# Kernel optimization log

Measured on AMD Instinct MI355X. Metric: run time of the kernel, lower is better.

The kernel has to match this reference:

```python
import jax, jax.numpy as jnp
import numpy as np

NUM_SHARED = 2
NUM_EXPERTS = 8
NUM_LOCAL = NUM_EXPERTS - NUM_SHARED
TOP_K = 2
BALANCE_COEFF = 0.1
INPUT_DIM = 256
HIDDEN_DIM = 512
PRED_LEN = 256
NUM_SCALES = 3


def _gelu(v):
    return jax.nn.gelu(v, approximate=False)  # torch nn.GELU default = exact erf


def setup_inputs() -> dict:
    key = jax.random.key(0)
    ks = iter(jax.random.split(key, 32))
    s = 0.02

    def w(shape):
        return jax.random.normal(next(ks), shape, dtype=jnp.float32) * s

    inp = {}
    inp["xs"] = jax.random.normal(next(ks), (NUM_SCALES, 32, 512, INPUT_DIM), dtype=jnp.float32)
    # router: Linear(E, 2E) -> GELU -> Linear(2E, num_experts) -> softmax
    inp["router_w1"] = w((INPUT_DIM, 2 * INPUT_DIM)); inp["router_b1"] = jnp.zeros((2 * INPUT_DIM,), jnp.float32)
    inp["router_w2"] = w((2 * INPUT_DIM, NUM_EXPERTS)); inp["router_b2"] = jnp.zeros((NUM_EXPERTS,), jnp.float32)
    # global experts (3-layer MLP), stacked over num_shared
    inp["gW1"] = w((NUM_SHARED, INPUT_DIM, HIDDEN_DIM)); inp["gb1"] = jnp.zeros((NUM_SHARED, HIDDEN_DIM), jnp.float32)
    inp["gW2"] = w((NUM_SHARED, HIDDEN_DIM, HIDDEN_DIM)); inp["gb2"] = jnp.zeros((NUM_SHARED, HIDDEN_DIM), jnp.float32)
    inp["gW3"] = w((NUM_SHARED, HIDDEN_DIM, PRED_LEN)); inp["gb3"] = jnp.zeros((NUM_SHARED, PRED_LEN), jnp.float32)
    # local experts (2-layer MLP), stacked over num_local
    inp["lW1"] = w((NUM_LOCAL, INPUT_DIM, HIDDEN_DIM)); inp["lb1"] = jnp.zeros((NUM_LOCAL, HIDDEN_DIM), jnp.float32)
    inp["lW2"] = w((NUM_LOCAL, HIDDEN_DIM, PRED_LEN)); inp["lb2"] = jnp.zeros((NUM_LOCAL, PRED_LEN), jnp.float32)
    # TemporalAwareWeighting
    inp["te_w"] = w((PRED_LEN, PRED_LEN)); inp["te_b"] = jnp.zeros((PRED_LEN,), jnp.float32)
    inp["weight_memory"] = jnp.zeros((1, NUM_SCALES), jnp.float32)
    inp["wc_w"] = w((PRED_LEN * NUM_SCALES + NUM_SCALES, NUM_SCALES)); inp["wc_b"] = jnp.zeros((NUM_SCALES,), jnp.float32)
    # output layer
    inp["out_w1"] = w((PRED_LEN, PRED_LEN)); inp["out_b1"] = jnp.zeros((PRED_LEN,), jnp.float32)
    inp["out_w2"] = w((PRED_LEN, PRED_LEN)); inp["out_b2"] = jnp.zeros((PRED_LEN,), jnp.float32)
    return inp


def reference(xs, router_w1, router_b1, router_w2, router_b2,
              gW1, gb1, gW2, gb2, gW3, gb3,
              lW1, lb1, lW2, lb2,
              te_w, te_b, weight_memory, wc_w, wc_b,
              out_w1, out_b1, out_w2, out_b2):
    S, B, C, E = xs.shape
    x = xs.reshape(S, B * C, E)

    def scale_fwd(xf):  # xf: [T, E]
        h = _gelu(xf @ router_w1 + router_b1)
        w = jax.nn.softmax(h @ router_w2 + router_b2, axis=-1)  # [T, Ne]
        gw = w[:, :NUM_SHARED]
        lw, lidx = jax.lax.top_k(w[:, NUM_SHARED:], TOP_K)      # sorted desc, like torch.topk
        # global experts: all run, weighted sum
        gh = _gelu(jnp.einsum('te,seh->sth', xf, gW1) + gb1[:, None, :])
        gh = _gelu(jnp.einsum('sth,shg->stg', gh, gW2) + gb2[:, None, :])
        gout = jnp.einsum('stg,sgo->sto', gh, gW3) + gb3[:, None, :]   # [Ns, T, O]
        global_pred = jnp.einsum('sto,ts->to', gout, gw)
        # local experts: all run (as in source), then top-k gather
        lh = _gelu(jnp.einsum('te,neh->nth', xf, lW1) + lb1[:, None, :])
        lout = jnp.einsum('nth,nho->nto', lh, lW2) + lb2[:, None, :]   # [Nl, T, O]
        sel = jnp.take_along_axis(jnp.swapaxes(lout, 0, 1), lidx[:, :, None], axis=1)  # [T, k, O]
        local_pred = jnp.sum(sel * lw[:, :, None], axis=1)
        return global_pred + local_pred, w

    preds, all_w = jax.vmap(scale_fwd)(x)  # [S, T, O], [S, T, Ne]

    ws = all_w.reshape(-1, all_w.shape[-1])
    entropy = -jnp.mean(jnp.sum(ws * jnp.log(ws + 1e-8), axis=-1))
    balance_loss = BALANCE_COEFF * entropy

    preds_bc = preds.reshape(S, B, C, -1)
    # TemporalAwareWeighting (dropout = identity in eval)
    reprs = _gelu(jnp.mean(preds_bc, axis=2) @ te_w + te_b)            # [S, B, O]
    concat = jnp.transpose(reprs, (1, 0, 2)).reshape(B, -1)            # [B, S*O]
    mem = jnp.broadcast_to(weight_memory, (B, S))
    raw = jax.nn.softplus(jnp.tanh(jnp.concatenate([concat, mem], axis=-1) @ wc_w + wc_b))
    sw = jax.nn.softmax(raw, axis=-1)                                  # [B, S]

    weighted = jnp.einsum('sbco,bs->bco', preds_bc, sw)
    out = _gelu(weighted @ out_w1 + out_b1) @ out_w2 + out_b2
    return out, balance_loss
```

## Files before the change

kernel.cpp:

```cpp
#include <hip/hip_runtime.h>
#include <hip/hip_bf16.h>
#include <math.h>

#define S_   3
#define B_   32
#define C_   512
#define E_   256
#define H_   512
#define P_   256
#define T_   49152
#define TBC_ 16384

typedef __attribute__((ext_vector_type(8))) short v_s16x8;
typedef __attribute__((ext_vector_type(4))) float v_f32x4;

__device__ __forceinline__ float gelu_f(float x) {
  return 0.5f * x * (1.0f + erff(x * 0.70710678118654752440f));
}

__device__ __forceinline__ void gload_lds16(const void* g, void* l) {
  __builtin_amdgcn_global_load_lds((const __attribute__((address_space(1))) void*)g,
                                   (__attribute__((address_space(3))) void*)l, 16, 0, 0);
}

template<int MODE, bool STORE, bool SPLITA>
__global__ __launch_bounds__(256)
void gemm_bf16_k(const __hip_bfloat16* __restrict__ A,
                 const __hip_bfloat16* __restrict__ Bt,
                 const float* __restrict__ bias,
                 void* __restrict__ Cout,
                 const float* __restrict__ wtok,
                 int M, int N, int K, int eidxBase,
                 const __hip_bfloat16* __restrict__ Alo,
                 int lda, int ldb, int ldc,
                 __hip_bfloat16* __restrict__ Gout,
                 const float* __restrict__ Ball)
{
  __shared__ __align__(16) unsigned short As[4096];
  __shared__ __align__(16) unsigned short Bs[4096];
  __shared__ float BallS[(MODE == 6 && STORE) ? 2048 : 1];
  const int tid  = threadIdx.x;
  const int wid  = tid >> 6;
  const int lane = tid & 63;
  const int wm = wid >> 1, wn = wid & 1;
  const int l15 = lane & 15, l4 = lane >> 4;

  if constexpr (MODE == 6 && STORE) {
    for (int i = tid; i < 2048; i += 256) BallS[i] = Ball[i];
  }

  v_f32x4 acc[4][4] = {};

  const size_t ArsB = (size_t)lda * 2;
  const size_t BrsB = (size_t)ldb * 2;
  const char* AgHi = (const char*)A + (size_t)blockIdx.x * 128 * ArsB;
  const char* AgLo = SPLITA ? ((const char*)Alo + (size_t)blockIdx.x * 128 * ArsB) : nullptr;
  const char* Bg   = (const char*)Bt + (size_t)blockIdx.y * 128 * BrsB;

  const int ob0 = (0 * 4 + wid) * 1024 + lane * 16;
  const int ob1 = (1 * 4 + wid) * 1024 + lane * 16;
  const int r0 = ob0 >> 6, kb0 = ob0 & 63;
  const int r1 = ob1 >> 6, kb1 = ob1 & 63;
  char* lA0 = (char*)As + (0 * 4 + wid) * 1024;
  char* lA1 = (char*)As + (1 * 4 + wid) * 1024;
  char* lB0 = (char*)Bs + (0 * 4 + wid) * 1024;
  char* lB1 = (char*)Bs + (1 * 4 + wid) * 1024;
  const size_t aoff0 = (size_t)r0 * ArsB + kb0;
  const size_t aoff1 = (size_t)r1 * ArsB + kb1;
  const char* gB0 = Bg + (size_t)r0 * BrsB + kb0;
  const char* gB1 = Bg + (size_t)r1 * BrsB + kb1;

  for (int kt = 0; kt < K; kt += 32) {
    const char* Asrc = AgHi;
    size_t akt = (size_t)kt * 2;
    if (SPLITA) {
      akt = (size_t)(kt & 255) * 2;
      if ((kt >> 8) == 1) Asrc = AgLo;
    }
    size_t bkt = (size_t)kt * 2;
    gload_lds16(Asrc + aoff0 + akt, lA0);
    gload_lds16(Asrc + aoff1 + akt, lA1);
    gload_lds16(gB0 + bkt, lB0);
    gload_lds16(gB1 + bkt, lB1);
    __syncthreads();
    v_s16x8 af[4], bfv[4];
#pragma unroll
    for (int m = 0; m < 4; ++m)
      af[m] = *(const v_s16x8*)(As + (wm * 64 + m * 16 + l15) * 32 + l4 * 8);
#pragma unroll
    for (int n = 0; n < 4; ++n)
      bfv[n] = *(const v_s16x8*)(Bs + (wn * 64 + n * 16 + l15) * 32 + l4 * 8);
#pragma unroll
    for (int m = 0; m < 4; ++m)
#pragma unroll
      for (int n = 0; n < 4; ++n)
        acc[m][n] = __builtin_amdgcn_mfma_f32_16x16x32_bf16(af[m], bfv[n], acc[m][n], 0, 0, 0);
    __syncthreads();
  }

  const int crow0 = blockIdx.x * 128 + wm * 64;
  const int ccol0 = blockIdx.y * 128 + wn * 64;

  if constexpr (MODE == 6) {
    float* P = (float*)Cout;
#pragma unroll
    for (int m = 0; m < 4; ++m) {
      float4 w0[4], w1[4];
      if (STORE) {
#pragma unroll
        for (int j = 0; j < 4; ++j) {
          const float4* wp = (const float4*)&wtok[(size_t)(crow0 + m * 16 + l4 * 4 + j) * 8];
          w0[j] = wp[0]; w1[j] = wp[1];
        }
      }
#pragma unroll
      for (int n = 0; n < 4; ++n) {
        const int col = ccol0 + n * 16 + l15;
        float bs[8];
        if (STORE) {
#pragma unroll
          for (int e = 0; e < 8; ++e) bs[e] = BallS[e * 256 + col];
        }
#pragma unroll
        for (int j = 0; j < 4; ++j) {
          const int row = crow0 + m * 16 + l4 * 4 + j;
          float v = acc[m][n][j];
          if (STORE) {
            v += bs[0] * w0[j].x + bs[1] * w0[j].y + bs[2] * w0[j].z + bs[3] * w0[j].w
               + bs[4] * w1[j].x + bs[5] * w1[j].y + bs[6] * w1[j].z + bs[7] * w1[j].w;
            P[(size_t)row * ldc + col] = v;
          } else {
            P[(size_t)row * ldc + col] += v;
          }
        }
      }
    }
    return;
  }

#pragma unroll
  for (int m = 0; m < 4; ++m) {
    float wv[4];
    if (MODE == 1 || MODE == 4 || MODE == 7) {
      int e4 = 0;
      if (MODE == 1) e4 = eidxBase;
      if (MODE == 4) e4 = eidxBase + (ccol0 >> 9);
      if (MODE == 7) e4 = (ccol0 >> 9);
#pragma unroll
      for (int j = 0; j < 4; ++j)
        wv[j] = wtok[(size_t)(crow0 + m * 16 + l4 * 4 + j) * 8 + e4];
    }
#pragma unroll
    for (int n = 0; n < 4; ++n) {
      const int col = ccol0 + n * 16 + l15;
      const float bv = bias[col];
#pragma unroll
      for (int j = 0; j < 4; ++j) {
        const int row = crow0 + m * 16 + l4 * 4 + j;
        float v = acc[m][n][j] + bv;
        if constexpr (MODE == 0) {
          ((__hip_bfloat16*)Cout)[(size_t)row * ldc + col] = __float2bfloat16(gelu_f(v));
        } else if constexpr (MODE == 1) {
          float* Pp = (float*)Cout + (size_t)row * ldc + col;
          float val = v * wv[j];
          if (STORE) *Pp = val; else *Pp += val;
        } else if constexpr (MODE == 2) {
          ((float*)Cout)[(size_t)row * ldc + col] = v;
        } else if constexpr (MODE == 3) {
          ((float*)Cout)[(size_t)row * ldc + col] = gelu_f(v);
        } else if constexpr (MODE == 4) {
          ((__hip_bfloat16*)Cout)[(size_t)row * ldc + col] = __float2bfloat16(wv[j] * gelu_f(v));
        } else if constexpr (MODE == 7) {
          if (ccol0 < 1024) {
            Gout[(size_t)row * 1024 + col] = __float2bfloat16(gelu_f(v));
          } else {
            ((__hip_bfloat16*)Cout)[(size_t)row * ldc + col] = __float2bfloat16(wv[j] * gelu_f(v));
          }
        }
      }
    }
  }
}

__global__ __launch_bounds__(256) void logits_kernel(
    const float* __restrict__ hr,
    const float* __restrict__ w2,
    const float* __restrict__ b2,
    float* __restrict__ wtok,
    float* __restrict__ entp)
{
  const int t = blockIdx.x * 256 + threadIdx.x;
  const float4* hrow = (const float4*)(hr + (size_t)t * 512);
  float lg[8];
#pragma unroll
  for (int e = 0; e < 8; ++e) lg[e] = b2[e];
#pragma unroll 4
  for (int k4 = 0; k4 < 128; ++k4) {
    float4 hv = hrow[k4];
    float hvv[4] = {hv.x, hv.y, hv.z, hv.w};
#pragma unroll
    for (int j = 0; j < 4; ++j) {
      const float* wr = w2 + (k4 * 4 + j) * 8;
#pragma unroll
      for (int e = 0; e < 8; ++e) lg[e] += hvv[j] * wr[e];
    }
  }
  float we[8];
  float mx = lg[0];
#pragma unroll
  for (int e = 1; e < 8; ++e) mx = fmaxf(mx, lg[e]);
  float ssum = 0.f;
#pragma unroll
  for (int e = 0; e < 8; ++e) { we[e] = expf(lg[e] - mx); ssum += we[e]; }
#pragma unroll
  for (int e = 0; e < 8; ++e) we[e] = we[e] / ssum;
  float ent = 0.f;
#pragma unroll
  for (int e = 0; e < 8; ++e) ent += we[e] * logf(we[e] + 1e-8f);
  int i1 = 0; float v1 = we[2];
#pragma unroll
  for (int n = 1; n < 6; ++n) if (we[2 + n] > v1) { v1 = we[2 + n]; i1 = n; }
  int i2 = -1; float v2 = -1e30f;
#pragma unroll
  for (int n = 0; n < 6; ++n) if (n != i1 && we[2 + n] > v2) { v2 = we[2 + n]; i2 = n; }
  float ow[8];
  ow[0] = we[0]; ow[1] = we[1];
#pragma unroll
  for (int n = 0; n < 6; ++n) ow[2 + n] = 0.f;
  ow[2 + i1] = v1; ow[2 + i2] = v2;
  float* wp = wtok + (size_t)t * 8;
#pragma unroll
  for (int e = 0; e < 8; ++e) wp[e] = ow[e];
  __shared__ float red[256];
  red[threadIdx.x] = ent;
  __syncthreads();
  for (int s = 128; s > 0; s >>= 1) {
    if (threadIdx.x < s) red[threadIdx.x] += red[threadIdx.x + s];
    __syncthreads();
  }
  if (threadIdx.x == 0) atomicAdd(entp, red[0]);
}

__global__ void zero_kernel(float* p) { p[0] = 0.f; }

__global__ void convert_x_kernel(const float* __restrict__ x,
                                 __hip_bfloat16* __restrict__ xb,
                                 __hip_bfloat16* __restrict__ xlo, int n4) {
  int stride = gridDim.x * blockDim.x;
  for (int i = blockIdx.x * blockDim.x + threadIdx.x; i < n4; i += stride) {
    float4 v = ((const float4*)x)[i];
    float vv[4] = {v.x, v.y, v.z, v.w};
    union { __hip_bfloat16 h[4]; ushort4 u; } hi, lo;
#pragma unroll
    for (int j = 0; j < 4; ++j) {
      hi.h[j] = __float2bfloat16(vv[j]);
      lo.h[j] = __float2bfloat16(vv[j] - __bfloat162float(hi.h[j]));
    }
    ((ushort4*)xb)[i] = hi.u;
    ((ushort4*)xlo)[i] = lo.u;
  }
}

__global__ void build_router_w_kernel(const float* __restrict__ rw1,
                                      __hip_bfloat16* __restrict__ dst) {
  int i = blockIdx.x * 256 + threadIdx.x;
  int n = i / 768, k = i - n * 768;
  float src = rw1[(size_t)(k & 255) * 512 + n];
  __hip_bfloat16 hv = __float2bfloat16(src);
  dst[i] = (k < 512) ? hv : __float2bfloat16(src - __bfloat162float(hv));
}

__global__ void build_biases_kernel(const float* __restrict__ gb1, const float* __restrict__ lb1,
                                    const float* __restrict__ gb3, const float* __restrict__ lb2,
                                    float* __restrict__ biasA, float* __restrict__ biasB,
                                    float* __restrict__ Ball) {
  int i = blockIdx.x * 256 + threadIdx.x;
  if (i < 2048) {
    biasA[i] = (i < 1024) ? gb1[i] : lb1[i - 1024];
  } else if (i < 4096) {
    int j = i - 2048;
    biasB[j] = lb1[1024 + j];
  } else {
    int j = i - 4096;
    Ball[j] = (j < 512) ? gb3[j] : lb2[j - 512];
  }
}

struct ConvDesc { const float* src; __hip_bfloat16* dst; int K; int N; int ldb; int koff; };
struct ConvArgs { ConvDesc d[20]; };

__global__ void convert_wt_kernel(ConvArgs a) {
  ConvDesc c = a.d[blockIdx.y];
  int total = c.K * c.N;
  int stride = gridDim.x * blockDim.x;
  for (int e = blockIdx.x * blockDim.x + threadIdx.x; e < total; e += stride) {
    int n = e / c.K;
    int k = e - n * c.K;
    c.dst[(size_t)n * c.ldb + c.koff + k] = __float2bfloat16(c.src[(size_t)k * c.N + n]);
  }
}

__global__ void mean_kernel(const float* __restrict__ pred, float* __restrict__ meanz) {
  int r = blockIdx.x, o = threadIdx.x;
  const float* p = pred + (size_t)r * 512 * 256 + o;
  float s0 = 0.f, s1 = 0.f, s2 = 0.f, s3 = 0.f;
  for (int c = 0; c < 512; c += 4) {
    s0 += p[(size_t)(c + 0) * 256]; s1 += p[(size_t)(c + 1) * 256];
    s2 += p[(size_t)(c + 2) * 256]; s3 += p[(size_t)(c + 3) * 256];
  }
  meanz[r * 256 + o] = (s0 + s1 + s2 + s3) * (1.0f / 512.0f);
}

__global__ void te_kernel(const float* __restrict__ meanz, const float* __restrict__ tw,
                          const float* __restrict__ tb, float* __restrict__ reprs) {
  __shared__ float row[256];
  int r = blockIdx.x, j = threadIdx.x;
  row[j] = meanz[r * 256 + j];
  __syncthreads();
  float a = 0.f;
  for (int k = 0; k < 256; ++k) a += row[k] * tw[k * 256 + j];
  reprs[r * 256 + j] = gelu_f(a + tb[j]);
}

__global__ void wc_kernel(const float* __restrict__ reprs, const float* __restrict__ wmem,
                          const float* __restrict__ wcw, const float* __restrict__ wcb,
                          float* __restrict__ sw) {
  __shared__ float red[128][3];
  int b = blockIdx.x, tid = threadIdx.x;
  float a0 = 0.f, a1 = 0.f, a2 = 0.f;
  for (int i = tid; i < 771; i += 128) {
    float cv = (i < 768) ? reprs[(i >> 8) * 8192 + b * 256 + (i & 255)] : wmem[i - 768];
    a0 += cv * wcw[i * 3 + 0]; a1 += cv * wcw[i * 3 + 1]; a2 += cv * wcw[i * 3 + 2];
  }
  red[tid][0] = a0; red[tid][1] = a1; red[tid][2] = a2;
  __syncthreads();
  for (int s = 64; s > 0; s >>= 1) {
    if (tid < s) {
      red[tid][0] += red[tid + s][0];
      red[tid][1] += red[tid + s][1];
      red[tid][2] += red[tid + s][2];
    }
    __syncthreads();
  }
  if (tid == 0) {
    float r[3]; float mx = -1e30f;
    for (int j = 0; j < 3; ++j) {
      float v = tanhf(red[0][j] + wcb[j]);
      r[j] = log1pf(expf(v));
      mx = fmaxf(mx, r[j]);
    }
    float s = 0.f;
    for (int j = 0; j < 3; ++j) { r[j] = expf(r[j] - mx); s += r[j]; }
    for (int j = 0; j < 3; ++j) sw[b * 3 + j] = r[j] / s;
  }
}

__global__ void weighted_kernel(const float* __restrict__ pred, const float* __restrict__ sw,
                                __hip_bfloat16* __restrict__ wb) {
  int t = blockIdx.x, o = threadIdx.x;
  int b = t >> 9;
  float s0 = sw[b * 3 + 0], s1 = sw[b * 3 + 1], s2 = sw[b * 3 + 2];
  size_t i = (size_t)t * 256 + o;
  float v = pred[i] * s0 + pred[i + (size_t)TBC_ * 256] * s1 + pred[i + (size_t)2 * TBC_ * 256] * s2;
  wb[i] = __float2bfloat16(v);
}

__global__ void finalize_kernel(const float* __restrict__ entp, float* __restrict__ out) {
  out[4194304] = -0.1f * entp[0] / 49152.0f;
}

extern "C" void kernel_launch(void* const* d_in, const int* in_sizes, int n_in,
                              void* d_out, int out_size, void* d_ws, size_t ws_size,
                              hipStream_t stream) {
  const float* x    = (const float*)d_in[0];
  const float* rw1  = (const float*)d_in[1];
  const float* rb1  = (const float*)d_in[2];
  const float* rw2  = (const float*)d_in[3];
  const float* rb2  = (const float*)d_in[4];
  const float* gW1  = (const float*)d_in[5];
  const float* gb1  = (const float*)d_in[6];
  const float* gW2  = (const float*)d_in[7];
  const float* gb2  = (const float*)d_in[8];
  const float* gW3  = (const float*)d_in[9];
  const float* gb3  = (const float*)d_in[10];
  const float* lW1  = (const float*)d_in[11];
  const float* lb1  = (const float*)d_in[12];
  const float* lW2  = (const float*)d_in[13];
  const float* lb2  = (const float*)d_in[14];
  const float* tew  = (const float*)d_in[15];
  const float* teb  = (const float*)d_in[16];
  const float* wmem = (const float*)d_in[17];
  const float* wcw  = (const float*)d_in[18];
  const float* wcb  = (const float*)d_in[19];
  const float* ow1  = (const float*)d_in[20];
  const float* ob1  = (const float*)d_in[21];
  const float* ow2  = (const float*)d_in[22];
  const float* ob2  = (const float*)d_in[23];
  float* out = (float*)d_out;

  char* ws = (char*)d_ws;
  size_t off = 0;
  auto alloc = [&](size_t bytes) -> void* {
    void* p = ws + off;
    off = (off + bytes + 255) & ~(size_t)255;
    return p;
  };

  const bool batched = (ws_size >= (440ull << 20));

  __hip_bfloat16* Xb   = (__hip_bfloat16*)alloc((size_t)T_ * E_ * 2);
  __hip_bfloat16* Xlo  = (__hip_bfloat16*)alloc((size_t)T_ * E_ * 2);
  __hip_bfloat16* rW1s = (__hip_bfloat16*)alloc(512ull * 768 * 2);
  float* wtok  = (float*)alloc((size_t)T_ * 8 * 4);
  float* entp  = (float*)alloc(256);
  float* meanz = (float*)alloc(96ull * 256 * 4);
  float* reprs = (float*)alloc(96ull * 256 * 4);
  float* swp   = (float*)alloc(512);
  __hip_bfloat16* ow1t = (__hip_bfloat16*)alloc((size_t)P_ * E_ * 2);
  __hip_bfloat16* ow2t = (__hip_bfloat16*)alloc((size_t)P_ * P_ * 2);

  zero_kernel<<<1, 1, 0, stream>>>(entp);
  convert_x_kernel<<<1024, 256, 0, stream>>>(x, Xb, Xlo, T_ * E_ / 4);
  build_router_w_kernel<<<1536, 256, 0, stream>>>(rw1, rW1s);

  if (batched) {
    __hip_bfloat16* Bt1a = (__hip_bfloat16*)alloc(2048ull * 256 * 2);
    __hip_bfloat16* Bt1b = (__hip_bfloat16*)alloc(2048ull * 256 * 2);
    __hip_bfloat16* gW2t = (__hip_bfloat16*)alloc(2ull * H_ * H_ * 2);
    __hip_bfloat16* Bf1  = (__hip_bfloat16*)alloc(256ull * 2048 * 2);
    __hip_bfloat16* Bf2  = (__hip_bfloat16*)alloc(256ull * 2048 * 2);
    float* biasA = (float*)alloc(2048 * 4);
    float* biasB = (float*)alloc(2048 * 4);
    float* Ball  = (float*)alloc(2048 * 4);
    __hip_bfloat16* Ap = (__hip_bfloat16*)alloc((size_t)T_ * 2048 * 2);
    __hip_bfloat16* G  = (__hip_bfloat16*)alloc((size_t)T_ * 1024 * 2);
    float* pred = (float*)alloc((size_t)T_ * P_ * 4);
    float* Hr = (float*)Ap;
    __hip_bfloat16* wghtB = Xlo;
    __hip_bfloat16* out1B = Xlo + (size_t)TBC_ * 256;

    ConvArgs ca;
    int d = 0;
    for (int s = 0; s < 2; ++s) ca.d[d++] = { gW1 + (size_t)s * E_ * H_, Bt1a + (size_t)s * 512 * 256, E_, H_, 256, 0 };
    for (int n = 0; n < 2; ++n) ca.d[d++] = { lW1 + (size_t)n * E_ * H_, Bt1a + (size_t)(2 + n) * 512 * 256, E_, H_, 256, 0 };
    for (int n = 2; n < 6; ++n) ca.d[d++] = { lW1 + (size_t)n * E_ * H_, Bt1b + (size_t)(n - 2) * 512 * 256, E_, H_, 256, 0 };
    for (int s = 0; s < 2; ++s) ca.d[d++] = { gW2 + (size_t)s * H_ * H_, gW2t + (size_t)s * H_ * H_, H_, H_, 512, 0 };
    for (int s = 0; s < 2; ++s) ca.d[d++] = { gW3 + (size_t)s * H_ * P_, Bf1, H_, P_, 2048, s * 512 };
    for (int n = 0; n < 2; ++n) ca.d[d++] = { lW2 + (size_t)n * H_ * P_, Bf1, H_, P_, 2048, (2 + n) * 512 };
    for (int n = 2; n < 6; ++n) ca.d[d++] = { lW2 + (size_t)n * H_ * P_, Bf2, H_, P_, 2048, (n - 2) * 512 };
    ca.d[d++] = { ow1, ow1t, E_, P_, 256, 0 };
    ca.d[d++] = { ow2, ow2t, P_, P_, 256, 0 };
    convert_wt_kernel<<<dim3(64, d), 256, 0, stream>>>(ca);
    build_biases_kernel<<<24, 256, 0, stream>>>(gb1, lb1, gb3, lb2, biasA, biasB, Ball);

    gemm_bf16_k<3, true, true><<<dim3(T_ / 128, 4), 256, 0, stream>>>(
        Xb, rW1s, rb1, Hr, nullptr, T_, 512, 768, 0, Xlo, 256, 768, 512, nullptr, nullptr);
    logits_kernel<<<T_ / 256, 256, 0, stream>>>(Hr, rw2, rb2, wtok, entp);

    gemm_bf16_k<7, true, false><<<dim3(T_ / 128, 16), 256, 0, stream>>>(
        Xb, Bt1a, biasA, Ap, wtok, T_, 2048, 256, 0, nullptr, 256, 256, 2048, G, nullptr);
    for (int s = 0; s < 2; ++s)
      gemm_bf16_k<4, true, false><<<dim3(T_ / 128, 4), 256, 0, stream>>>(
          G + (size_t)s * 512, gW2t + (size_t)s * H_ * H_, gb2 + s * H_,
          Ap + (size_t)s * 512, wtok, T_, 512, 512, s, nullptr, 1024, 512, 2048, nullptr, nullptr);
    gemm_bf16_k<6, true, false><<<dim3(T_ / 128, 2), 256, 0, stream>>>(
        Ap, Bf1, nullptr, pred, wtok, T_, 256, 2048, 0, nullptr, 2048, 2048, 256, nullptr, Ball);
    gemm_bf16_k<4, true, false><<<dim3(T_ / 128, 16), 256, 0, stream>>>(
        Xb, Bt1b, biasB, Ap, wtok, T_, 2048, 256, 4, nullptr, 256, 256, 2048, nullptr, nullptr);
    gemm_bf16_k<6, false, false><<<dim3(T_ / 128, 2), 256, 0, stream>>>(
        Ap, Bf2, nullptr, pred, wtok, T_, 256, 2048, 0, nullptr, 2048, 2048, 256, nullptr, nullptr);

    mean_kernel<<<96, 256, 0, stream>>>(pred, meanz);
    te_kernel<<<96, 256, 0, stream>>>(meanz, tew, teb, reprs);
    wc_kernel<<<32, 128, 0, stream>>>(reprs, wmem, wcw, wcb, swp);
    weighted_kernel<<<TBC_, 256, 0, stream>>>(pred, swp, wghtB);

    gemm_bf16_k<0, true, false><<<dim3(TBC_ / 128, 2), 256, 0, stream>>>(
        wghtB, ow1t, ob1, out1B, nullptr, TBC_, 256, 256, 0, nullptr, 256, 256, 256, nullptr, nullptr);
    gemm_bf16_k<2, true, false><<<dim3(TBC_ / 128, 2), 256, 0, stream>>>(
        out1B, ow2t, ob2, out, nullptr, TBC_, 256, 256, 0, nullptr, 256, 256, 256, nullptr, nullptr);
  } else {
    __hip_bfloat16* gW1t = (__hip_bfloat16*)alloc(2ull * H_ * E_ * 2);
    __hip_bfloat16* gW2t = (__hip_bfloat16*)alloc(2ull * H_ * H_ * 2);
    __hip_bfloat16* gW3t = (__hip_bfloat16*)alloc(2ull * P_ * H_ * 2);
    __hip_bfloat16* lW1t = (__hip_bfloat16*)alloc(6ull * H_ * E_ * 2);
    __hip_bfloat16* lW2t = (__hip_bfloat16*)alloc(6ull * P_ * H_ * 2);
    __hip_bfloat16* bufA = (__hip_bfloat16*)alloc((size_t)T_ * H_ * 2);
    __hip_bfloat16* bufB = (__hip_bfloat16*)alloc((size_t)T_ * H_ * 2);
    float* pred = (float*)alloc((size_t)T_ * P_ * 4);
    float* Hr = (float*)bufB;
    __hip_bfloat16* wghtB = bufA;
    __hip_bfloat16* out1B = bufB;

    ConvArgs ca;
    int d = 0;
    for (int s = 0; s < 2; ++s) ca.d[d++] = { gW1 + (size_t)s * E_ * H_, gW1t + (size_t)s * H_ * E_, E_, H_, 256, 0 };
    for (int s = 0; s < 2; ++s) ca.d[d++] = { gW2 + (size_t)s * H_ * H_, gW2t + (size_t)s * H_ * H_, H_, H_, 512, 0 };
    for (int s = 0; s < 2; ++s) ca.d[d++] = { gW3 + (size_t)s * H_ * P_, gW3t + (size_t)s * P_ * H_, H_, P_, 512, 0 };
    for (int n = 0; n < 6; ++n) ca.d[d++] = { lW1 + (size_t)n * E_ * H_, lW1t + (size_t)n * H_ * E_, E_, H_, 256, 0 };
    for (int n = 0; n < 6; ++n) ca.d[d++] = { lW2 + (size_t)n * H_ * P_, lW2t + (size_t)n * P_ * H_, H_, P_, 512, 0 };
    ca.d[d++] = { ow1, ow1t, E_, P_, 256, 0 };
    ca.d[d++] = { ow2, ow2t, P_, P_, 256, 0 };
    convert_wt_kernel<<<dim3(64, d), 256, 0, stream>>>(ca);

    gemm_bf16_k<3, true, true><<<dim3(T_ / 128, 4), 256, 0, stream>>>(
        Xb, rW1s, rb1, Hr, nullptr, T_, 512, 768, 0, Xlo, 256, 768, 512, nullptr, nullptr);
    logits_kernel<<<T_ / 256, 256, 0, stream>>>(Hr, rw2, rb2, wtok, entp);

    for (int s = 0; s < 2; ++s) {
      gemm_bf16_k<0, true, false><<<dim3(T_ / 128, 4), 256, 0, stream>>>(
          Xb, gW1t + (size_t)s * H_ * E_, gb1 + s * H_, bufA, nullptr, T_, 512, 256, 0, nullptr, 256, 256, 512, nullptr, nullptr);
      gemm_bf16_k<0, true, false><<<dim3(T_ / 128, 4), 256, 0, stream>>>(
          bufA, gW2t + (size_t)s * H_ * H_, gb2 + s * H_, bufB, nullptr, T_, 512, 512, 0, nullptr, 512, 512, 512, nullptr, nullptr);
      if (s == 0)
        gemm_bf16_k<1, true, false><<<dim3(T_ / 128, 2), 256, 0, stream>>>(
            bufB, gW3t + (size_t)s * P_ * H_, gb3 + s * P_, pred, wtok, T_, 256, 512, s, nullptr, 512, 512, 256, nullptr, nullptr);
      else
        gemm_bf16_k<1, false, false><<<dim3(T_ / 128, 2), 256, 0, stream>>>(
            bufB, gW3t + (size_t)s * P_ * H_, gb3 + s * P_, pred, wtok, T_, 256, 512, s, nullptr, 512, 512, 256, nullptr, nullptr);
    }
    for (int n = 0; n < 6; ++n) {
      gemm_bf16_k<0, true, false><<<dim3(T_ / 128, 4), 256, 0, stream>>>(
          Xb, lW1t + (size_t)n * H_ * E_, lb1 + n * H_, bufA, nullptr, T_, 512, 256, 0, nullptr, 256, 256, 512, nullptr, nullptr);
      gemm_bf16_k<1, false, false><<<dim3(T_ / 128, 2), 256, 0, stream>>>(
          bufA, lW2t + (size_t)n * P_ * H_, lb2 + n * P_, pred, wtok, T_, 256, 512, 2 + n, nullptr, 512, 512, 256, nullptr, nullptr);
    }

    mean_kernel<<<96, 256, 0, stream>>>(pred, meanz);
    te_kernel<<<96, 256, 0, stream>>>(meanz, tew, teb, reprs);
    wc_kernel<<<32, 128, 0, stream>>>(reprs, wmem, wcw, wcb, swp);
    weighted_kernel<<<TBC_, 256, 0, stream>>>(pred, swp, wghtB);

    gemm_bf16_k<0, true, false><<<dim3(TBC_ / 128, 2), 256, 0, stream>>>(
        wghtB, ow1t, ob1, out1B, nullptr, TBC_, 256, 256, 0, nullptr, 256, 256, 256, nullptr, nullptr);
    gemm_bf16_k<2, true, false><<<dim3(TBC_ / 128, 2), 256, 0, stream>>>(
        out1B, ow2t, ob2, out, nullptr, TBC_, 256, 256, 0, nullptr, 256, 256, 256, nullptr, nullptr);
  }

  finalize_kernel<<<1, 1, 0, stream>>>(entp, out);
  (void)in_sizes; (void)n_in; (void)out_size;
}
```

Baseline: 1.017 ms.

## Fuse router logits into first GEMM and pair experts to cut workspace

The router's second linear layer is folded into the first router GEMM's epilogue. Each block applies GELU, multiplies by the 512x8 router weights held in LDS, reduces across lanes with shuffles, and atomically adds partial logits into a zeroed wtok buffer. This removes the fp32 hidden-activation write and re-read. The two code paths (batched for large workspace, per-expert otherwise) are replaced by one schedule. That schedule processes global experts in half-token chunks into a 1024-wide packed buffer, then runs local experts two at a time (N=1024 up-projection, K=1024 fused down-projection). This reduces workspace and launch count versus the fallback path, at the cost of more launches than the old batched path and float atomics that make the logit summation order nondeterministic.

```diff
diff --git a/kernel.cpp b/kernel.cpp
--- a/kernel.cpp
+++ b/kernel.cpp
@@ -33,20 +33,22 @@
                  int M, int N, int K, int eidxBase,
                  const __hip_bfloat16* __restrict__ Alo,
                  int lda, int ldb, int ldc,
-                 __hip_bfloat16* __restrict__ Gout,
                  const float* __restrict__ Ball)
 {
   __shared__ __align__(16) unsigned short As[4096];
   __shared__ __align__(16) unsigned short Bs[4096];
-  __shared__ float BallS[(MODE == 6 && STORE) ? 2048 : 1];
+  __shared__ float XtraS[(MODE == 8) ? 4608 : ((MODE == 6 && STORE) ? 2048 : 1)];
   const int tid  = threadIdx.x;
   const int wid  = tid >> 6;
   const int lane = tid & 63;
   const int wm = wid >> 1, wn = wid & 1;
   const int l15 = lane & 15, l4 = lane >> 4;
 
-  if constexpr (MODE == 6 && STORE) {
-    for (int i = tid; i < 2048; i += 256) BallS[i] = Ball[i];
+  if constexpr (MODE == 8) {
+    for (int i = tid; i < 4096; i += 256) XtraS[i] = Ball[i];
+    for (int i = tid; i < 512; i += 256) XtraS[4096 + i] = bias[i];
+  } else if constexpr (MODE == 6 && STORE) {
+    for (int i = tid; i < 2048; i += 256) XtraS[i] = Ball[i];
   }
 
   v_f32x4 acc[4][4] = {};
@@ -101,6 +103,37 @@
   const int crow0 = blockIdx.x * 128 + wm * 64;
   const int ccol0 = blockIdx.y * 128 + wn * 64;
 
+  if constexpr (MODE == 8) {
+    float* Lg = (float*)Cout;
+#pragma unroll
+    for (int m = 0; m < 4; ++m) {
+#pragma unroll
+      for (int j = 0; j < 4; ++j) {
+        float pe[8];
+#pragma unroll
+        for (int e = 0; e < 8; ++e) pe[e] = 0.f;
+#pragma unroll
+        for (int n = 0; n < 4; ++n) {
+          const int col = ccol0 + n * 16 + l15;
+          const float h = gelu_f(acc[m][n][j] + XtraS[4096 + col]);
+          const float* w2r = &XtraS[col * 8];
+#pragma unroll
+          for (int e = 0; e < 8; ++e) pe[e] += h * w2r[e];
+        }
+#pragma unroll
+        for (int off = 1; off < 16; off <<= 1)
+#pragma unroll
+          for (int e = 0; e < 8; ++e) pe[e] += __shfl_xor(pe[e], off);
+        if (l15 == 0) {
+          const int row = crow0 + m * 16 + l4 * 4 + j;
+#pragma unroll
+          for (int e = 0; e < 8; ++e) atomicAdd(&Lg[(size_t)row * 8 + e], pe[e]);
+        }
+      }
+    }
+    return;
+  }
+
   if constexpr (MODE == 6) {
     float* P = (float*)Cout;
 #pragma unroll
@@ -119,7 +152,7 @@
         float bs[8];
         if (STORE) {
 #pragma unroll
-          for (int e = 0; e < 8; ++e) bs[e] = BallS[e * 256 + col];
+          for (int e = 0; e < 8; ++e) bs[e] = XtraS[e * 256 + col];
         }
 #pragma unroll
         for (int j = 0; j < 4; ++j) {
@@ -141,11 +174,8 @@
 #pragma unroll
   for (int m = 0; m < 4; ++m) {
     float wv[4];
-    if (MODE == 1 || MODE == 4 || MODE == 7) {
-      int e4 = 0;
-      if (MODE == 1) e4 = eidxBase;
-      if (MODE == 4) e4 = eidxBase + (ccol0 >> 9);
-      if (MODE == 7) e4 = (ccol0 >> 9);
+    if (MODE == 4) {
+      const int e4 = eidxBase + (ccol0 >> 9);
 #pragma unroll
       for (int j = 0; j < 4; ++j)
         wv[j] = wtok[(size_t)(crow0 + m * 16 + l4 * 4 + j) * 8 + e4];
@@ -160,52 +190,23 @@
         float v = acc[m][n][j] + bv;
         if constexpr (MODE == 0) {
           ((__hip_bfloat16*)Cout)[(size_t)row * ldc + col] = __float2bfloat16(gelu_f(v));
-        } else if constexpr (MODE == 1) {
-          float* Pp = (float*)Cout + (size_t)row * ldc + col;
-          float val = v * wv[j];
-          if (STORE) *Pp = val; else *Pp += val;
         } else if constexpr (MODE == 2) {
           ((float*)Cout)[(size_t)row * ldc + col] = v;
-        } else if constexpr (MODE == 3) {
-          ((float*)Cout)[(size_t)row * ldc + col] = gelu_f(v);
         } else if constexpr (MODE == 4) {
           ((__hip_bfloat16*)Cout)[(size_t)row * ldc + col] = __float2bfloat16(wv[j] * gelu_f(v));
-        } else if constexpr (MODE == 7) {
-          if (ccol0 < 1024) {
-            Gout[(size_t)row * 1024 + col] = __float2bfloat16(gelu_f(v));
-          } else {
-            ((__hip_bfloat16*)Cout)[(size_t)row * ldc + col] = __float2bfloat16(wv[j] * gelu_f(v));
-          }
         }
       }
     }
   }
 }
 
-__global__ __launch_bounds__(256) void logits_kernel(
-    const float* __restrict__ hr,
-    const float* __restrict__ w2,
-    const float* __restrict__ b2,
-    float* __restrict__ wtok,
-    float* __restrict__ entp)
-{
+__global__ __launch_bounds__(256) void logits_finish_kernel(
+    float* __restrict__ wtok, const float* __restrict__ b2, float* __restrict__ entp) {
   const int t = blockIdx.x * 256 + threadIdx.x;
-  const float4* hrow = (const float4*)(hr + (size_t)t * 512);
-  float lg[8];
-#pragma unroll
-  for (int e = 0; e < 8; ++e) lg[e] = b2[e];
-#pragma unroll 4
-  for (int k4 = 0; k4 < 128; ++k4) {
-    float4 hv = hrow[k4];
-    float hvv[4] = {hv.x, hv.y, hv.z, hv.w};
-#pragma unroll
-    for (int j = 0; j < 4; ++j) {
-      const float* wr = w2 + (k4 * 4 + j) * 8;
-#pragma unroll
-      for (int e = 0; e < 8; ++e) lg[e] += hvv[j] * wr[e];
-    }
-  }
-  float we[8];
+  float* wp = wtok + (size_t)t * 8;
+  float lg[8], we[8];
+#pragma unroll
+  for (int e = 0; e < 8; ++e) lg[e] = wp[e] + b2[e];
   float mx = lg[0];
 #pragma unroll
   for (int e = 1; e < 8; ++e) mx = fmaxf(mx, lg[e]);
@@ -228,7 +229,6 @@
 #pragma unroll
   for (int n = 0; n < 6; ++n) ow[2 + n] = 0.f;
   ow[2 + i1] = v1; ow[2 + i2] = v2;
-  float* wp = wtok + (size_t)t * 8;
 #pragma unroll
   for (int e = 0; e < 8; ++e) wp[e] = ow[e];
   __shared__ float red[256];
@@ -241,7 +241,11 @@
   if (threadIdx.x == 0) atomicAdd(entp, red[0]);
 }
 
-__global__ void zero_kernel(float* p) { p[0] = 0.f; }
+__global__ void zero_wtok_kernel(float4* __restrict__ w, float* __restrict__ entp) {
+  const int i = blockIdx.x * 256 + threadIdx.x;
+  w[i] = make_float4(0.f, 0.f, 0.f, 0.f);
+  if (i == 0) entp[0] = 0.f;
+}
 
 __global__ void convert_x_kernel(const float* __restrict__ x,
                                  __hip_bfloat16* __restrict__ xb,
@@ -270,20 +274,10 @@
   dst[i] = (k < 512) ? hv : __float2bfloat16(src - __bfloat162float(hv));
 }
 
-__global__ void build_biases_kernel(const float* __restrict__ gb1, const float* __restrict__ lb1,
-                                    const float* __restrict__ gb3, const float* __restrict__ lb2,
-                                    float* __restrict__ biasA, float* __restrict__ biasB,
-                                    float* __restrict__ Ball) {
+__global__ void build_ball_kernel(const float* __restrict__ gb3, const float* __restrict__ lb2,
+                                  float* __restrict__ Ball) {
   int i = blockIdx.x * 256 + threadIdx.x;
-  if (i < 2048) {
-    biasA[i] = (i < 1024) ? gb1[i] : lb1[i - 1024];
-  } else if (i < 4096) {
-    int j = i - 2048;
-    biasB[j] = lb1[1024 + j];
-  } else {
-    int j = i - 4096;
-    Ball[j] = (j < 512) ? gb3[j] : lb2[j - 512];
-  }
+  Ball[i] = (i < 512) ? gb3[i] : lb2[i - 512];
 }
 
 struct ConvDesc { const float* src; __hip_bfloat16* dst; int K; int N; int ldb; int koff; };
@@ -405,138 +399,88 @@
     off = (off + bytes + 255) & ~(size_t)255;
     return p;
   };
-
-  const bool batched = (ws_size >= (440ull << 20));
-
-  __hip_bfloat16* Xb   = (__hip_bfloat16*)alloc((size_t)T_ * E_ * 2);
-  __hip_bfloat16* Xlo  = (__hip_bfloat16*)alloc((size_t)T_ * E_ * 2);
-  __hip_bfloat16* rW1s = (__hip_bfloat16*)alloc(512ull * 768 * 2);
+  __hip_bfloat16* Xb    = (__hip_bfloat16*)alloc((size_t)T_ * E_ * 2);
+  __hip_bfloat16* Xlo   = (__hip_bfloat16*)alloc((size_t)T_ * E_ * 2);
+  __hip_bfloat16* rW1s  = (__hip_bfloat16*)alloc(512ull * 768 * 2);
   float* wtok  = (float*)alloc((size_t)T_ * 8 * 4);
   float* entp  = (float*)alloc(256);
   float* meanz = (float*)alloc(96ull * 256 * 4);
   float* reprs = (float*)alloc(96ull * 256 * 4);
   float* swp   = (float*)alloc(512);
-  __hip_bfloat16* ow1t = (__hip_bfloat16*)alloc((size_t)P_ * E_ * 2);
-  __hip_bfloat16* ow2t = (__hip_bfloat16*)alloc((size_t)P_ * P_ * 2);
-
-  zero_kernel<<<1, 1, 0, stream>>>(entp);
+  __hip_bfloat16* ow1t  = (__hip_bfloat16*)alloc((size_t)P_ * E_ * 2);
+  __hip_bfloat16* ow2t  = (__hip_bfloat16*)alloc((size_t)P_ * P_ * 2);
+  __hip_bfloat16* gW1t  = (__hip_bfloat16*)alloc(2ull * H_ * E_ * 2);
+  __hip_bfloat16* gW2t  = (__hip_bfloat16*)alloc(2ull * H_ * H_ * 2);
+  __hip_bfloat16* BfG   = (__hip_bfloat16*)alloc(256ull * 1024 * 2);
+  __hip_bfloat16* lW1tP = (__hip_bfloat16*)alloc(3ull * 1024 * 256 * 2);
+  __hip_bfloat16* BfL   = (__hip_bfloat16*)alloc(3ull * 256 * 1024 * 2);
+  float* Ball  = (float*)alloc(2048 * 4);
+  __hip_bfloat16* bufP  = (__hip_bfloat16*)alloc((size_t)T_ * 1024 * 2);
+  float* pred  = (float*)alloc((size_t)T_ * P_ * 4);
+
+  __hip_bfloat16* gh1h  = Xlo;
+  __hip_bfloat16* wghtB = Xlo;
+  __hip_bfloat16* out1B = Xlo + (size_t)TBC_ * 256;
+
+  ConvArgs ca;
+  int d = 0;
+  for (int s = 0; s < 2; ++s)
+    ca.d[d++] = { gW1 + (size_t)s * E_ * H_, gW1t + (size_t)s * 512 * 256, E_, H_, 256, 0 };
+  for (int s = 0; s < 2; ++s)
+    ca.d[d++] = { gW2 + (size_t)s * H_ * H_, gW2t + (size_t)s * 512 * 512, H_, H_, 512, 0 };
+  for (int s = 0; s < 2; ++s)
+    ca.d[d++] = { gW3 + (size_t)s * H_ * P_, BfG, H_, P_, 1024, s * 512 };
+  for (int e = 0; e < 6; ++e)
+    ca.d[d++] = { lW1 + (size_t)e * E_ * H_, lW1tP + (size_t)(e >> 1) * 1024 * 256 + (size_t)(e & 1) * 512 * 256,
+                  E_, H_, 256, 0 };
+  for (int e = 0; e < 6; ++e)
+    ca.d[d++] = { lW2 + (size_t)e * H_ * P_, BfL + (size_t)(e >> 1) * 256 * 1024, H_, P_, 1024, (e & 1) * 512 };
+  ca.d[d++] = { ow1, ow1t, E_, P_, 256, 0 };
+  ca.d[d++] = { ow2, ow2t, P_, P_, 256, 0 };
+
+  zero_wtok_kernel<<<384, 256, 0, stream>>>((float4*)wtok, entp);
   convert_x_kernel<<<1024, 256, 0, stream>>>(x, Xb, Xlo, T_ * E_ / 4);
   build_router_w_kernel<<<1536, 256, 0, stream>>>(rw1, rW1s);
-
-  if (batched) {
-    __hip_bfloat16* Bt1a = (__hip_bfloat16*)alloc(2048ull * 256 * 2);
-    __hip_bfloat16* Bt1b = (__hip_bfloat16*)alloc(2048ull * 256 * 2);
-    __hip_bfloat16* gW2t = (__hip_bfloat16*)alloc(2ull * H_ * H_ * 2);
-    __hip_bfloat16* Bf1  = (__hip_bfloat16*)alloc(256ull * 2048 * 2);
-    __hip_bfloat16* Bf2  = (__hip_bfloat16*)alloc(256ull * 2048 * 2);
-    float* biasA = (float*)alloc(2048 * 4);
-    float* biasB = (float*)alloc(2048 * 4);
-    float* Ball  = (float*)alloc(2048 * 4);
-    __hip_bfloat16* Ap = (__hip_bfloat16*)alloc((size_t)T_ * 2048 * 2);
-    __hip_bfloat16* G  = (__hip_bfloat16*)alloc((size_t)T_ * 1024 * 2);
-    float* pred = (float*)alloc((size_t)T_ * P_ * 4);
-    float* Hr = (float*)Ap;
-    __hip_bfloat16* wghtB = Xlo;
-    __hip_bfloat16* out1B = Xlo + (size_t)TBC_ * 256;
-
-    ConvArgs ca;
-    int d = 0;
-    for (int s = 0; s < 2; ++s) ca.d[d++] = { gW1 + (size_t)s * E_ * H_, Bt1a + (size_t)s * 512 * 256, E_, H_, 256, 0 };
-    for (int n = 0; n < 2; ++n) ca.d[d++] = { lW1 + (size_t)n * E_ * H_, Bt1a + (size_t)(2 + n) * 512 * 256, E_, H_, 256, 0 };
-    for (int n = 2; n < 6; ++n) ca.d[d++] = { lW1 + (size_t)n * E_ * H_, Bt1b + (size_t)(n - 2) * 512 * 256, E_, H_, 256, 0 };
-    for (int s = 0; s < 2; ++s) ca.d[d++] = { gW2 + (size_t)s * H_ * H_, gW2t + (size_t)s * H_ * H_, H_, H_, 512, 0 };
-    for (int s = 0; s < 2; ++s) ca.d[d++] = { gW3 + (size_t)s * H_ * P_, Bf1, H_, P_, 2048, s * 512 };
-    for (int n = 0; n < 2; ++n) ca.d[d++] = { lW2 + (size_t)n * H_ * P_, Bf1, H_, P_, 2048, (2 + n) * 512 };
-    for (int n = 2; n < 6; ++n) ca.d[d++] = { lW2 + (size_t)n * H_ * P_, Bf2, H_, P_, 2048, (n - 2) * 512 };
-    ca.d[d++] = { ow1, ow1t, E_, P_, 256, 0 };
-    ca.d[d++] = { ow2, ow2t, P_, P_, 256, 0 };
-    convert_wt_kernel<<<dim3(64, d), 256, 0, stream>>>(ca);
-    build_biases_kernel<<<24, 256, 0, stream>>>(gb1, lb1, gb3, lb2, biasA, biasB, Ball);
-
-    gemm_bf16_k<3, true, true><<<dim3(T_ / 128, 4), 256, 0, stream>>>(
-        Xb, rW1s, rb1, Hr, nullptr, T_, 512, 768, 0, Xlo, 256, 768, 512, nullptr, nullptr);
-    logits_kernel<<<T_ / 256, 256, 0, stream>>>(Hr, rw2, rb2, wtok, entp);
-
-    gemm_bf16_k<7, true, false><<<dim3(T_ / 128, 16), 256, 0, stream>>>(
-        Xb, Bt1a, biasA, Ap, wtok, T_, 2048, 256, 0, nullptr, 256, 256, 2048, G, nullptr);
-    for (int s = 0; s < 2; ++s)
-      gemm_bf16_k<4, true, false><<<dim3(T_ / 128, 4), 256, 0, stream>>>(
-          G + (size_t)s * 512, gW2t + (size_t)s * H_ * H_, gb2 + s * H_,
-          Ap + (size_t)s * 512, wtok, T_, 512, 512, s, nullptr, 1024, 512, 2048, nullptr, nullptr);
-    gemm_bf16_k<6, true, false><<<dim3(T_ / 128, 2), 256, 0, stream>>>(
-        Ap, Bf1, nullptr, pred, wtok, T_, 256, 2048, 0, nullptr, 2048, 2048, 256, nullptr, Ball);
-    gemm_bf16_k<4, true, false><<<dim3(T_ / 128, 16), 256, 0, stream>>>(
-        Xb, Bt1b, biasB, Ap, wtok, T_, 2048, 256, 4, nullptr, 256, 256, 2048, nullptr, nullptr);
+  convert_wt_kernel<<<dim3(64, 20), 256, 0, stream>>>(ca);
+  build_ball_kernel<<<8, 256, 0, stream>>>(gb3, lb2, Ball);
+
+  gemm_bf16_k<8, true, true><<<dim3(T_ / 128, 4), 256, 0, stream>>>(
+      Xb, rW1s, rb1, wtok, nullptr, T_, 512, 768, 0, Xlo, 256, 768, 0, rw2);
+  logits_finish_kernel<<<T_ / 256, 256, 0, stream>>>(wtok, rb2, entp);
+
+  for (int s = 0; s < 2; ++s) {
+    for (int half = 0; half < 2; ++half) {
+      const size_t r0 = (size_t)half * (T_ / 2);
+      gemm_bf16_k<0, true, false><<<dim3(T_ / 256, 4), 256, 0, stream>>>(
+          Xb + r0 * 256, gW1t + (size_t)s * 512 * 256, gb1 + s * 512, gh1h, nullptr,
+          T_ / 2, 512, 256, 0, nullptr, 256, 256, 512, nullptr);
+      gemm_bf16_k<4, true, false><<<dim3(T_ / 256, 4), 256, 0, stream>>>(
+          gh1h, gW2t + (size_t)s * 512 * 512, gb2 + s * 512, bufP + r0 * 1024 + s * 512,
+          wtok + r0 * 8, T_ / 2, 512, 512, s, nullptr, 512, 512, 1024, nullptr);
+    }
+  }
+  gemm_bf16_k<6, true, false><<<dim3(T_ / 128, 2), 256, 0, stream>>>(
+      bufP, BfG, nullptr, pred, wtok, T_, 256, 1024, 0, nullptr, 1024, 1024, 256, Ball);
+
+  for (int p = 0; p < 3; ++p) {
+    gemm_bf16_k<4, true, false><<<dim3(T_ / 128, 8), 256, 0, stream>>>(
+        Xb, lW1tP + (size_t)p * 1024 * 256, lb1 + p * 1024, bufP, wtok,
+        T_, 1024, 256, 2 + 2 * p, nullptr, 256, 256, 1024, nullptr);
     gemm_bf16_k<6, false, false><<<dim3(T_ / 128, 2), 256, 0, stream>>>(
-        Ap, Bf2, nullptr, pred, wtok, T_, 256, 2048, 0, nullptr, 2048, 2048, 256, nullptr, nullptr);
-
-    mean_kernel<<<96, 256, 0, stream>>>(pred, meanz);
-    te_kernel<<<96, 256, 0, stream>>>(meanz, tew, teb, reprs);
-    wc_kernel<<<32, 128, 0, stream>>>(reprs, wmem, wcw, wcb, swp);
-    weighted_kernel<<<TBC_, 256, 0, stream>>>(pred, swp, wghtB);
-
-    gemm_bf16_k<0, true, false><<<dim3(TBC_ / 128, 2), 256, 0, stream>>>(
-        wghtB, ow1t, ob1, out1B, nullptr, TBC_, 256, 256, 0, nullptr, 256, 256, 256, nullptr, nullptr);
-    gemm_bf16_k<2, true, false><<<dim3(TBC_ / 128, 2), 256, 0, stream>>>(
-        out1B, ow2t, ob2, out, nullptr, TBC_, 256, 256, 0, nullptr, 256, 256, 256, nullptr, nullptr);
-  } else {
-    __hip_bfloat16* gW1t = (__hip_bfloat16*)alloc(2ull * H_ * E_ * 2);
-    __hip_bfloat16* gW2t = (__hip_bfloat16*)alloc(2ull * H_ * H_ * 2);
-    __hip_bfloat16* gW3t = (__hip_bfloat16*)alloc(2ull * P_ * H_ * 2);
-    __hip_bfloat16* lW1t = (__hip_bfloat16*)alloc(6ull * H_ * E_ * 2);
-    __hip_bfloat16* lW2t = (__hip_bfloat16*)alloc(6ull * P_ * H_ * 2);
-    __hip_bfloat16* bufA = (__hip_bfloat16*)alloc((size_t)T_ * H_ * 2);
-    __hip_bfloat16* bufB = (__hip_bfloat16*)alloc((size_t)T_ * H_ * 2);
-    float* pred = (float*)alloc((size_t)T_ * P_ * 4);
-    float* Hr = (float*)bufB;
-    __hip_bfloat16* wghtB = bufA;
-    __hip_bfloat16* out1B = bufB;
-
-    ConvArgs ca;
-    int d = 0;
-    for (int s = 0; s < 2; ++s) ca.d[d++] = { gW1 + (size_t)s * E_ * H_, gW1t + (size_t)s * H_ * E_, E_, H_, 256, 0 };
-    for (int s = 0; s < 2; ++s) ca.d[d++] = { gW2 + (size_t)s * H_ * H_, gW2t + (size_t)s * H_ * H_, H_, H_, 512, 0 };
-    for (int s = 0; s < 2; ++s) ca.d[d++] = { gW3 + (size_t)s * H_ * P_, gW3t + (size_t)s * P_ * H_, H_, P_, 512, 0 };
-    for (int n = 0; n < 6; ++n) ca.d[d++] = { lW1 + (size_t)n * E_ * H_, lW1t + (size_t)n * H_ * E_, E_, H_, 256, 0 };
-    for (int n = 0; n < 6; ++n) ca.d[d++] = { lW2 + (size_t)n * H_ * P_, lW2t + (size_t)n * P_ * H_, H_, P_, 512, 0 };
-    ca.d[d++] = { ow1, ow1t, E_, P_, 256, 0 };
-    ca.d[d++] = { ow2, ow2t, P_, P_, 256, 0 };
-    convert_wt_kernel<<<dim3(64, d), 256, 0, stream>>>(ca);
-
-    gemm_bf16_k<3, true, true><<<dim3(T_ / 128, 4), 256, 0, stream>>>(
-        Xb, rW1s, rb1, Hr, nullptr, T_, 512, 768, 0, Xlo, 256, 768, 512, nullptr, nullptr);
-    logits_kernel<<<T_ / 256, 256, 0, stream>>>(Hr, rw2, rb2, wtok, entp);
-
-    for (int s = 0; s < 2; ++s) {
-      gemm_bf16_k<0, true, false><<<dim3(T_ / 128, 4), 256, 0, stream>>>(
-          Xb, gW1t + (size_t)s * H_ * E_, gb1 + s * H_, bufA, nullptr, T_, 512, 256, 0, nullptr, 256, 256, 512, nullptr, nullptr);
-      gemm_bf16_k<0, true, false><<<dim3(T_ / 128, 4), 256, 0, stream>>>(
-          bufA, gW2t + (size_t)s * H_ * H_, gb2 + s * H_, bufB, nullptr, T_, 512, 512, 0, nullptr, 512, 512, 512, nullptr, nullptr);
-      if (s == 0)
-        gemm_bf16_k<1, true, false><<<dim3(T_ / 128, 2), 256, 0, stream>>>(
-            bufB, gW3t + (size_t)s * P_ * H_, gb3 + s * P_, pred, wtok, T_, 256, 512, s, nullptr, 512, 512, 256, nullptr, nullptr);
-      else
-        gemm_bf16_k<1, false, false><<<dim3(T_ / 128, 2), 256, 0, stream>>>(
-            bufB, gW3t + (size_t)s * P_ * H_, gb3 + s * P_, pred, wtok, T_, 256, 512, s, nullptr, 512, 512, 256, nullptr, nullptr);
-    }
-    for (int n = 0; n < 6; ++n) {
-      gemm_bf16_k<0, true, false><<<dim3(T_ / 128, 4), 256, 0, stream>>>(
-          Xb, lW1t + (size_t)n * H_ * E_, lb1 + n * H_, bufA, nullptr, T_, 512, 256, 0, nullptr, 256, 256, 512, nullptr, nullptr);
-      gemm_bf16_k<1, false, false><<<dim3(T_ / 128, 2), 256, 0, stream>>>(
-          bufA, lW2t + (size_t)n * P_ * H_, lb2 + n * P_, pred, wtok, T_, 256, 512, 2 + n, nullptr, 512, 512, 256, nullptr, nullptr);
-    }
-
-    mean_kernel<<<96, 256, 0, stream>>>(pred, meanz);
-    te_kernel<<<96, 256, 0, stream>>>(meanz, tew, teb, reprs);
-    wc_kernel<<<32, 128, 0, stream>>>(reprs, wmem, wcw, wcb, swp);
-    weighted_kernel<<<TBC_, 256, 0, stream>>>(pred, swp, wghtB);
-
-    gemm_bf16_k<0, true, false><<<dim3(TBC_ / 128, 2), 256, 0, stream>>>(
-        wghtB, ow1t, ob1, out1B, nullptr, TBC_, 256, 256, 0, nullptr, 256, 256, 256, nullptr, nullptr);
-    gemm_bf16_k<2, true, false><<<dim3(TBC_ / 128, 2), 256, 0, stream>>>(
-        out1B, ow2t, ob2, out, nullptr, TBC_, 256, 256, 0, nullptr, 256, 256, 256, nullptr, nullptr);
-  }
+        bufP, BfL + (size_t)p * 256 * 1024, nullptr, pred, wtok,
+        T_, 256, 1024, 0, nullptr, 1024, 1024, 256, nullptr);
+  }
+
+  mean_kernel<<<96, 256, 0, stream>>>(pred, meanz);
+  te_kernel<<<96, 256, 0, stream>>>(meanz, tew, teb, reprs);
+  wc_kernel<<<32, 128, 0, stream>>>(reprs, wmem, wcw, wcb, swp);
+  weighted_kernel<<<TBC_, 256, 0, stream>>>(pred, swp, wghtB);
+
+  gemm_bf16_k<0, true, false><<<dim3(TBC_ / 128, 2), 256, 0, stream>>>(
+      wghtB, ow1t, ob1, out1B, nullptr, TBC_, 256, 256, 0, nullptr, 256, 256, 256, nullptr);
+  gemm_bf16_k<2, true, false><<<dim3(TBC_ / 128, 2), 256, 0, stream>>>(
+      out1B, ow2t, ob2, out, nullptr, TBC_, 256, 256, 0, nullptr, 256, 256, 256, nullptr);
 
   finalize_kernel<<<1, 1, 0, stream>>>(entp, out);
-  (void)in_sizes; (void)n_in; (void)out_size;
-}
+  (void)in_sizes; (void)n_in; (void)out_size; (void)ws_size;
+}
```

Result: slower. 1.075 ms (+5.7%).
